# Optimization experiments

Hardware: AMD Instinct MI355X
Metric: run time of the kernel (lower is better)

Reference implementation:

```python
import jax, jax.numpy as jnp
import numpy as np

B, S, H, D = 8, 1024, 32, 128
SM_SCALE = D ** -0.5


def _make_bias(dtype=jnp.float32):
    # causal mask [1, 1, S, S]
    causal = jnp.tril(jnp.ones((S, S), dtype=bool))[None, None, :, :]
    attn_mask = jnp.ones((B, S), dtype=bool).at[:, S // 2:].set(False)
    pad = attn_mask[:, None, None, :]  # [B,1,1,S]
    combined = jnp.logical_and(causal, pad)  # [B,1,S,S]
    neg = jnp.finfo(dtype).min
    return jnp.where(combined, jnp.asarray(0.0, dtype), jnp.asarray(neg, dtype))


def setup_inputs() -> dict:
    key = jax.random.key(0)
    kq, kk, kv = jax.random.split(key, 3)
    query = jax.random.normal(kq, (B, S, H, D), dtype=jnp.float32)
    k = jax.random.normal(kk, (B, S, H, D), dtype=jnp.float32)
    v = jax.random.normal(kv, (B, S, H, D), dtype=jnp.float32)
    bias = _make_bias()
    return {"query": query, "key": k, "value": v, "bias": bias}


def reference(query, key, value, bias):
    # query/key/value: [B, S, H, D]; bias: [B, 1, Sq, Sk] (broadcast over heads)
    scores = jnp.einsum("bqhd,bkhd->bhqk", query, key) * SM_SCALE + bias
    attn = jax.nn.softmax(scores, axis=-1)
    out = jnp.einsum("bhqk,bkhd->bqhd", attn, value)
    return out
```

## Files before the change

kernel.cpp:

```cpp
#include <hip/hip_runtime.h>
#include <stdint.h>

typedef __attribute__((ext_vector_type(8))) short short8;
typedef __attribute__((ext_vector_type(4))) float f32x4;
typedef __attribute__((ext_vector_type(4))) unsigned short usvec4;

#define B_ 8
#define S_ 1024
#define H_ 32
#define D_ 128

static __device__ __forceinline__ unsigned short f2bf(float f) {
  uint32_t u = __builtin_bit_cast(uint32_t, f);
  u += 0x7FFFu + ((u >> 16) & 1u);
  return (unsigned short)(u >> 16);
}

__global__ __launch_bounds__(256, 2)
void fa_fwd(const float* __restrict__ Qp,
            const float* __restrict__ Kp,
            const float* __restrict__ Vp,
            const float* __restrict__ BiasP,
            float* __restrict__ Op)
{
  __shared__ __align__(16) unsigned short klds[32 * 136];
  __shared__ __align__(16) unsigned short vlds[8 * 520];

  const int tid  = threadIdx.x;
  const int lane = tid & 63;
  const int w    = tid >> 6;
  const int quad = lane >> 4;
  const int c    = lane & 15;

  const int qt = blockIdx.x;
  const int h  = blockIdx.y;
  const int b  = blockIdx.z;
  const int qi = qt * 64 + w * 16 + c;

  const size_t strideS = (size_t)H_ * D_;
  const size_t bh = ((size_t)b * S_) * strideS + (size_t)h * D_;

  short8 qf[4];
  {
    const float* qrow = Qp + bh + (size_t)qi * strideS;
#pragma unroll
    for (int f = 0; f < 4; ++f) {
      float4 a  = *(const float4*)(qrow + f * 32 + quad * 8);
      float4 bv = *(const float4*)(qrow + f * 32 + quad * 8 + 4);
      short8 r;
      r[0] = (short)f2bf(a.x);  r[1] = (short)f2bf(a.y);
      r[2] = (short)f2bf(a.z);  r[3] = (short)f2bf(a.w);
      r[4] = (short)f2bf(bv.x); r[5] = (short)f2bf(bv.y);
      r[6] = (short)f2bf(bv.z); r[7] = (short)f2bf(bv.w);
      qf[f] = r;
    }
  }

  const float* brow = BiasP + ((size_t)b * S_ + qi) * S_;
  const float NEGT = -1e37f;

  float m  = -INFINITY;
  float ll = 0.f;
  f32x4 acc[8];
#pragma unroll
  for (int t = 0; t < 8; ++t) acc[t] = (f32x4){0.f, 0.f, 0.f, 0.f};

  const float SL2E = 0.08838834764831845f * 1.4426950408889634f;
  const float L2E  = 1.4426950408889634f;

  for (int ks = 0; ks < S_; ks += 32) {
    float4 b0f = *(const float4*)(brow + ks + quad * 4);
    float4 b1f = *(const float4*)(brow + ks + 16 + quad * 4);
    float b0a[4] = {b0f.x, b0f.y, b0f.z, b0f.w};
    float b1a[4] = {b1f.x, b1f.y, b1f.z, b1f.w};
    int lv = 0;
#pragma unroll
    for (int r = 0; r < 4; ++r) lv |= (b0a[r] > NEGT) | (b1a[r] > NEGT);
    const int wv = __any(lv);
    const int bvalid = __syncthreads_or(wv);
    if (!bvalid) continue;

    {
      const int kk = tid >> 3;
      const int dc = tid & 7;

      const float* krow = Kp + bh + (size_t)(ks + kk) * strideS + dc * 16;
      unsigned short kb16[16];
#pragma unroll
      for (int i = 0; i < 4; ++i) {
        float4 kv = *(const float4*)(krow + i * 4);
        kb16[i*4+0] = f2bf(kv.x); kb16[i*4+1] = f2bf(kv.y);
        kb16[i*4+2] = f2bf(kv.z); kb16[i*4+3] = f2bf(kv.w);
      }
      usvec4* kdst = (usvec4*)(klds + kk * 136 + dc * 16);
#pragma unroll
      for (int i = 0; i < 4; ++i)
        kdst[i] = (usvec4){kb16[i*4+0], kb16[i*4+1], kb16[i*4+2], kb16[i*4+3]};

      const float* vrow = Vp + bh + (size_t)(ks + kk) * strideS + dc * 16;
      const int base = dc * 520 + (kk >> 3) * 128 + (kk & 7);
#pragma unroll
      for (int i = 0; i < 4; ++i) {
        float4 vv = *(const float4*)(vrow + i * 4);
        vlds[base + (i*4+0)*8] = f2bf(vv.x);
        vlds[base + (i*4+1)*8] = f2bf(vv.y);
        vlds[base + (i*4+2)*8] = f2bf(vv.z);
        vlds[base + (i*4+3)*8] = f2bf(vv.w);
      }
    }
    __syncthreads();

    if (wv) {
      f32x4 st0 = (f32x4){0.f, 0.f, 0.f, 0.f};
      f32x4 st1 = (f32x4){0.f, 0.f, 0.f, 0.f};
#pragma unroll
      for (int f = 0; f < 4; ++f) {
        short8 ka = *(const short8*)(klds + c * 136 + f * 32 + quad * 8);
        short8 kb = *(const short8*)(klds + (16 + c) * 136 + f * 32 + quad * 8);
        st0 = __builtin_amdgcn_mfma_f32_16x16x32_bf16(ka, qf[f], st0, 0, 0, 0);
        st1 = __builtin_amdgcn_mfma_f32_16x16x32_bf16(kb, qf[f], st1, 0, 0, 0);
      }

      float x0[4], x1[4];
      float mt = -INFINITY;
#pragma unroll
      for (int r = 0; r < 4; ++r) {
        x0[r] = (b0a[r] > NEGT) ? fmaf(b0a[r], L2E, st0[r] * SL2E) : -INFINITY;
        x1[r] = (b1a[r] > NEGT) ? fmaf(b1a[r], L2E, st1[r] * SL2E) : -INFINITY;
        mt = fmaxf(mt, fmaxf(x0[r], x1[r]));
      }
      mt = fmaxf(mt, __shfl_xor(mt, 16));
      mt = fmaxf(mt, __shfl_xor(mt, 32));
      const float mn    = fmaxf(m, mt);
      const float alpha = exp2f(m - mn);
      m = mn;

      float p0[4], p1[4];
      float lt = 0.f;
#pragma unroll
      for (int r = 0; r < 4; ++r) {
        p0[r] = exp2f(x0[r] - mn);
        p1[r] = exp2f(x1[r] - mn);
        lt += p0[r] + p1[r];
      }
      lt += __shfl_xor(lt, 16);
      lt += __shfl_xor(lt, 32);
      ll = ll * alpha + lt;

#pragma unroll
      for (int t = 0; t < 8; ++t) {
        acc[t][0] *= alpha; acc[t][1] *= alpha;
        acc[t][2] *= alpha; acc[t][3] *= alpha;
      }

      const int i0 = (int)(((uint32_t)f2bf(p0[0])) | ((uint32_t)f2bf(p0[1]) << 16));
      const int i1 = (int)(((uint32_t)f2bf(p0[2])) | ((uint32_t)f2bf(p0[3]) << 16));
      const int i2 = (int)(((uint32_t)f2bf(p1[0])) | ((uint32_t)f2bf(p1[1]) << 16));
      const int i3 = (int)(((uint32_t)f2bf(p1[2])) | ((uint32_t)f2bf(p1[3]) << 16));

      const int srcA = ((quad & 1) << 5) + c;
      const int srcB = srcA + 16;
      const int hiT  = quad >> 1;

      int sA, sB, w0, w1, w2, w3;
      sA = __shfl(i0, srcA); sB = __shfl(i2, srcA); w0 = hiT ? sB : sA;
      sA = __shfl(i1, srcA); sB = __shfl(i3, srcA); w1 = hiT ? sB : sA;
      sA = __shfl(i0, srcB); sB = __shfl(i2, srcB); w2 = hiT ? sB : sA;
      sA = __shfl(i1, srcB); sB = __shfl(i3, srcB); w3 = hiT ? sB : sA;

      union { int u[4]; short8 v; } pf;
      pf.u[0] = w0; pf.u[1] = w1; pf.u[2] = w2; pf.u[3] = w3;

#pragma unroll
      for (int t = 0; t < 8; ++t) {
        short8 vf = *(const short8*)(vlds + t * 520 + lane * 8);
        acc[t] = __builtin_amdgcn_mfma_f32_16x16x32_bf16(vf, pf.v, acc[t], 0, 0, 0);
      }
    }
    __syncthreads();
  }

  const float rl = 1.0f / ll;
  float* orow = Op + bh + (size_t)qi * strideS;
#pragma unroll
  for (int t = 0; t < 8; ++t) {
    float4 o;
    o.x = acc[t][0] * rl; o.y = acc[t][1] * rl;
    o.z = acc[t][2] * rl; o.w = acc[t][3] * rl;
    *(float4*)(orow + t * 16 + quad * 4) = o;
  }
}

extern "C" void kernel_launch(void* const* d_in, const int* in_sizes, int n_in,
                              void* d_out, int out_size, void* d_ws, size_t ws_size,
                              hipStream_t stream) {
  const float* q    = (const float*)d_in[0];
  const float* k    = (const float*)d_in[1];
  const float* v    = (const float*)d_in[2];
  const float* bias = (const float*)d_in[3];
  float* out = (float*)d_out;

  dim3 grid(S_ / 64, H_, B_);
  fa_fwd<<<grid, 256, 0, stream>>>(q, k, v, bias, out);
}
```

Baseline: 626.4 us.

## Pre-pack K/V to bf16 MFMA layout and compress bias into bitmask

Adds pre-kernels that convert K and V to bf16, already laid out in MFMA fragment order, and that compress the fp32 bias into per-row 32-bit validity masks. A new attention kernel loads these tiles straight into LDS with global_load_lds into double buffers, with one barrier per step. It also skips the rescale while the running max grows only a little, uses packed bf16 convert instructions, and raises wave priority around the MFMA blocks. The goal is to stop every block re-reading and re-converting fp32 K/V and the bias, at the cost of extra preprocessing passes and a large workspace. Treating the bias as a binary mask is only correct when bias values are exactly 0 or very negative, as in this benchmark.

```diff
diff --git a/kernel.cpp b/kernel.cpp
--- a/kernel.cpp
+++ b/kernel.cpp
@@ -2,6 +2,7 @@
 #include <stdint.h>
 
 typedef __attribute__((ext_vector_type(8))) short short8;
+typedef __attribute__((ext_vector_type(8))) unsigned short us8;
 typedef __attribute__((ext_vector_type(4))) float f32x4;
 typedef __attribute__((ext_vector_type(4))) unsigned short usvec4;
 
@@ -9,11 +10,237 @@
 #define S_ 1024
 #define H_ 32
 #define D_ 128
+#define NSTEP (S_ / 32)
 
 static __device__ __forceinline__ unsigned short f2bf(float f) {
   uint32_t u = __builtin_bit_cast(uint32_t, f);
   u += 0x7FFFu + ((u >> 16) & 1u);
   return (unsigned short)(u >> 16);
+}
+
+__global__ __launch_bounds__(256)
+void kv_pre(const float* __restrict__ Kp, const float* __restrict__ Vp,
+            unsigned short* __restrict__ Kw, unsigned short* __restrict__ Vw)
+{
+  const int flat   = blockIdx.x * 256 + threadIdx.x;
+  const int tid2   = flat & 511;
+  const int bhstep = flat >> 9;
+  const int step   = bhstep & (NSTEP - 1);
+  const int bhi    = bhstep >> 5;
+  const int h      = bhi & (H_ - 1);
+  const int b      = bhi >> 5;
+
+  const size_t strideS = (size_t)H_ * D_;
+  const size_t base    = ((size_t)b * S_) * strideS + (size_t)h * D_;
+  const size_t dst     = (size_t)bhstep * 4096 + (size_t)tid2 * 8;
+
+  {
+    const int f = tid2 >> 7, tile = (tid2 >> 6) & 1, ln = tid2 & 63;
+    const int cc = ln & 15, qd = ln >> 4;
+    const float* src = Kp + base + (size_t)(step * 32 + tile * 16 + cc) * strideS + f * 32 + qd * 8;
+    float4 a = *(const float4*)src;
+    float4 c4 = *(const float4*)(src + 4);
+    us8 r;
+    r[0] = f2bf(a.x);  r[1] = f2bf(a.y);  r[2] = f2bf(a.z);  r[3] = f2bf(a.w);
+    r[4] = f2bf(c4.x); r[5] = f2bf(c4.y); r[6] = f2bf(c4.z); r[7] = f2bf(c4.w);
+    *(us8*)(Kw + dst) = r;
+  }
+  {
+    const int t = tid2 >> 6, ln = tid2 & 63;
+    const int cv = ln & 15, qv = ln >> 4;
+    const float* src = Vp + base + (size_t)(step * 32 + qv * 8) * strideS + t * 16 + cv;
+    us8 r;
+#pragma unroll
+    for (int j = 0; j < 8; ++j) r[j] = f2bf(src[(size_t)j * strideS]);
+    *(us8*)(Vw + dst) = r;
+  }
+}
+
+__global__ __launch_bounds__(256)
+void mask_pre(const float* __restrict__ BiasP, uint32_t* __restrict__ Mw)
+{
+  const int idx = blockIdx.x * 256 + threadIdx.x;
+  const float NEGT = -1e37f;
+  const float* src = BiasP + (size_t)idx * 32;
+  uint32_t mbits = 0;
+#pragma unroll
+  for (int j = 0; j < 8; ++j) {
+    float4 v = *(const float4*)(src + j * 4);
+    mbits |= (uint32_t)(v.x > NEGT) << (j * 4 + 0);
+    mbits |= (uint32_t)(v.y > NEGT) << (j * 4 + 1);
+    mbits |= (uint32_t)(v.z > NEGT) << (j * 4 + 2);
+    mbits |= (uint32_t)(v.w > NEGT) << (j * 4 + 3);
+  }
+  Mw[idx] = mbits;
+}
+
+__global__ __launch_bounds__(256, 2)
+void fa_fwd2(const float* __restrict__ Qp,
+             const unsigned short* __restrict__ Kw,
+             const unsigned short* __restrict__ Vw,
+             const uint32_t* __restrict__ Mw,
+             float* __restrict__ Op)
+{
+  __shared__ __align__(16) unsigned short klds[2][4096];
+  __shared__ __align__(16) unsigned short vlds[2][4096];
+
+  const int tid  = threadIdx.x;
+  const int lane = tid & 63;
+  const int w    = tid >> 6;
+  const int quad = lane >> 4;
+  const int c    = lane & 15;
+
+  const int qt = blockIdx.x;
+  const int h  = blockIdx.y;
+  const int b  = blockIdx.z;
+  const int qi = qt * 64 + w * 16 + c;
+
+  const size_t strideS = (size_t)H_ * D_;
+  const size_t bh  = ((size_t)b * S_) * strideS + (size_t)h * D_;
+  const size_t kvb = (size_t)(b * H_ + h) * ((size_t)NSTEP * 4096);
+
+  short8 qf[4];
+  {
+    const float* qrow = Qp + bh + (size_t)qi * strideS;
+#pragma unroll
+    for (int f = 0; f < 4; ++f) {
+      float4 a  = *(const float4*)(qrow + f * 32 + quad * 8);
+      float4 bv = *(const float4*)(qrow + f * 32 + quad * 8 + 4);
+      short8 r;
+      r[0] = (short)f2bf(a.x);  r[1] = (short)f2bf(a.y);
+      r[2] = (short)f2bf(a.z);  r[3] = (short)f2bf(a.w);
+      r[4] = (short)f2bf(bv.x); r[5] = (short)f2bf(bv.y);
+      r[6] = (short)f2bf(bv.z); r[7] = (short)f2bf(bv.w);
+      qf[f] = r;
+    }
+  }
+
+  const uint32_t* mrow = Mw + ((size_t)b * S_ + qi) * NSTEP;
+
+  float m  = -INFINITY;
+  float ll = 0.f;
+  f32x4 acc[8];
+#pragma unroll
+  for (int t = 0; t < 8; ++t) acc[t] = (f32x4){0.f, 0.f, 0.f, 0.f};
+
+  const float SL2E = 0.08838834764831845f * 1.4426950408889634f;
+  int cur = 0;
+
+  for (int st = 0; st < NSTEP; ++st) {
+    const uint32_t mw_ = mrow[st];
+    const int m0 = (mw_ >> (quad * 4)) & 15;
+    const int m1 = (mw_ >> (16 + quad * 4)) & 15;
+    const int wv = __any(m0 | m1);
+    const int bvalid = __syncthreads_or(wv);
+    if (!bvalid) continue;
+
+    {
+      const unsigned short* kg = Kw + kvb + (size_t)st * 4096 + w * 1024 + lane * 8;
+      const unsigned short* vg = Vw + kvb + (size_t)st * 4096 + w * 1024 + lane * 8;
+      unsigned short* kl = &klds[cur][w * 1024];
+      unsigned short* vl = &vlds[cur][w * 1024];
+#pragma unroll
+      for (int i = 0; i < 2; ++i) {
+        __builtin_amdgcn_global_load_lds(
+            (const __attribute__((address_space(1))) void*)(kg + i * 512),
+            (__attribute__((address_space(3))) void*)(kl + i * 512), 16, 0, 0);
+        __builtin_amdgcn_global_load_lds(
+            (const __attribute__((address_space(1))) void*)(vg + i * 512),
+            (__attribute__((address_space(3))) void*)(vl + i * 512), 16, 0, 0);
+      }
+    }
+    __syncthreads();
+
+    if (wv) {
+      const unsigned short* kb_ = klds[cur];
+      const unsigned short* vb_ = vlds[cur];
+
+      f32x4 st0 = (f32x4){0.f, 0.f, 0.f, 0.f};
+      f32x4 st1 = (f32x4){0.f, 0.f, 0.f, 0.f};
+      __builtin_amdgcn_s_setprio(1);
+#pragma unroll
+      for (int f = 0; f < 4; ++f) {
+        short8 ka  = *(const short8*)(kb_ + f * 1024 + lane * 8);
+        short8 kbt = *(const short8*)(kb_ + f * 1024 + 512 + lane * 8);
+        st0 = __builtin_amdgcn_mfma_f32_16x16x32_bf16(ka,  qf[f], st0, 0, 0, 0);
+        st1 = __builtin_amdgcn_mfma_f32_16x16x32_bf16(kbt, qf[f], st1, 0, 0, 0);
+      }
+      __builtin_amdgcn_s_setprio(0);
+
+      float x0[4], x1[4];
+      float mt = -INFINITY;
+#pragma unroll
+      for (int r = 0; r < 4; ++r) {
+        x0[r] = ((m0 >> r) & 1) ? st0[r] * SL2E : -INFINITY;
+        x1[r] = ((m1 >> r) & 1) ? st1[r] * SL2E : -INFINITY;
+        mt = fmaxf(mt, fmaxf(x0[r], x1[r]));
+      }
+      mt = fmaxf(mt, __shfl_xor(mt, 16));
+      mt = fmaxf(mt, __shfl_xor(mt, 32));
+
+      if (!__all(mt <= m + 8.f)) {
+        const float mn    = fmaxf(m, mt);
+        const float alpha = exp2f(m - mn);
+        m = mn;
+        ll *= alpha;
+#pragma unroll
+        for (int t = 0; t < 8; ++t) {
+          acc[t][0] *= alpha; acc[t][1] *= alpha;
+          acc[t][2] *= alpha; acc[t][3] *= alpha;
+        }
+      }
+
+      float p0[4], p1[4];
+      float lt = 0.f;
+#pragma unroll
+      for (int r = 0; r < 4; ++r) {
+        p0[r] = exp2f(x0[r] - m);
+        p1[r] = exp2f(x1[r] - m);
+        lt += p0[r] + p1[r];
+      }
+      lt += __shfl_xor(lt, 16);
+      lt += __shfl_xor(lt, 32);
+      ll += lt;
+
+      int i0, i1, i2, i3;
+      asm("v_cvt_pk_bf16_f32 %0, %1, %2" : "=v"(i0) : "v"(p0[0]), "v"(p0[1]));
+      asm("v_cvt_pk_bf16_f32 %0, %1, %2" : "=v"(i1) : "v"(p0[2]), "v"(p0[3]));
+      asm("v_cvt_pk_bf16_f32 %0, %1, %2" : "=v"(i2) : "v"(p1[0]), "v"(p1[1]));
+      asm("v_cvt_pk_bf16_f32 %0, %1, %2" : "=v"(i3) : "v"(p1[2]), "v"(p1[3]));
+
+      const int srcA = ((quad & 1) << 5) + c;
+      const int srcB = srcA + 16;
+      const int hiT  = quad >> 1;
+
+      int sA, sB, w0, w1, w2, w3;
+      sA = __shfl(i0, srcA); sB = __shfl(i2, srcA); w0 = hiT ? sB : sA;
+      sA = __shfl(i1, srcA); sB = __shfl(i3, srcA); w1 = hiT ? sB : sA;
+      sA = __shfl(i0, srcB); sB = __shfl(i2, srcB); w2 = hiT ? sB : sA;
+      sA = __shfl(i1, srcB); sB = __shfl(i3, srcB); w3 = hiT ? sB : sA;
+
+      union { int u[4]; short8 v; } pf;
+      pf.u[0] = w0; pf.u[1] = w1; pf.u[2] = w2; pf.u[3] = w3;
+
+      __builtin_amdgcn_s_setprio(1);
+#pragma unroll
+      for (int t = 0; t < 8; ++t) {
+        short8 vf = *(const short8*)(vb_ + t * 512 + lane * 8);
+        acc[t] = __builtin_amdgcn_mfma_f32_16x16x32_bf16(vf, pf.v, acc[t], 0, 0, 0);
+      }
+      __builtin_amdgcn_s_setprio(0);
+    }
+    cur ^= 1;
+  }
+
+  const float rl = 1.0f / ll;
+  float* orow = Op + bh + (size_t)qi * strideS;
+#pragma unroll
+  for (int t = 0; t < 8; ++t) {
+    float4 o;
+    o.x = acc[t][0] * rl; o.y = acc[t][1] * rl;
+    o.z = acc[t][2] * rl; o.w = acc[t][3] * rl;
+    *(float4*)(orow + t * 16 + quad * 4) = o;
+  }
 }
 
 __global__ __launch_bounds__(256, 2)
@@ -200,6 +427,19 @@
   const float* bias = (const float*)d_in[3];
   float* out = (float*)d_out;
 
+  const size_t KW_BYTES = (size_t)B_ * H_ * NSTEP * 4096 * 2;
+  const size_t MW_BYTES = (size_t)B_ * S_ * NSTEP * 4;
+  const size_t NEED     = 2 * KW_BYTES + MW_BYTES;
+
   dim3 grid(S_ / 64, H_, B_);
-  fa_fwd<<<grid, 256, 0, stream>>>(q, k, v, bias, out);
-}
+  if (ws_size >= NEED) {
+    unsigned short* Kw = (unsigned short*)d_ws;
+    unsigned short* Vw = (unsigned short*)((char*)d_ws + KW_BYTES);
+    uint32_t*       Mw = (uint32_t*)((char*)d_ws + 2 * KW_BYTES);
+    kv_pre<<<(B_ * H_ * NSTEP * 512) / 256, 256, 0, stream>>>(k, v, Kw, Vw);
+    mask_pre<<<(B_ * S_ * NSTEP) / 256, 256, 0, stream>>>(bias, Mw);
+    fa_fwd2<<<grid, 256, 0, stream>>>(q, Kw, Vw, Mw, out);
+  } else {
+    fa_fwd<<<grid, 256, 0, stream>>>(q, k, v, bias, out);
+  }
+}
```

Result: faster. 598.4 us (-4.5%).
